# Optimization experiments

Hardware: AMD Instinct MI355X
Metric: run time of the kernel (lower is better)

## Reference

```python
import jax, jax.numpy as jnp
import numpy as np

B = 8192          # batch size
D = 128           # embedding_dim
R = 1000          # relation_dict_len
MARGIN = 1.0


def setup_inputs() -> dict:
    key = jax.random.key(0)
    k1, k2, k3, k4 = jax.random.split(key, 4)
    return {
        "positive_batch": jax.random.normal(k1, (B, 3, D), dtype=jnp.float32),
        "negative_batch": jax.random.normal(k2, (B, 3, D), dtype=jnp.float32),
        "r_idx": jax.random.randint(k3, (B,), 0, R),
        "rel_emb": jax.random.normal(k4, (R, D * D), dtype=jnp.float32),
    }


def _score(batch, Wr):
    # batch: (B, 3, D) -> h, r, t each (B, D); Wr: (B, D, D)
    h, r, t = batch[:, 0], batch[:, 1], batch[:, 2]
    d = jnp.abs(h + r - t)                       # (B, D)
    # x^T Wr x quadratic form per example, fused in one einsum
    return jnp.einsum('bi,bij,bj->b', d, Wr, d)  # (B,)


def reference(positive_batch, negative_batch, r_idx, rel_emb):
    # Gather per-example relation matrix (Wr built from positive relation,
    # reused for the negative score, as in the original module).
    Wr = rel_emb[r_idx].reshape(-1, D, D)        # (B, D, D)
    pos = _score(positive_batch, Wr)
    neg = _score(negative_batch, Wr)
    return jnp.mean(jax.nn.relu(MARGIN + pos - neg))
```

## Files before the change

### kernel.cpp

```cpp
#include <hip/hip_runtime.h>

#define BATCH 8192
#define DIM 128
#define NREL 1000
#define MARGIN 1.0f

#define WS_PARTIAL 0
#define WS_CNT     8192
#define WS_PSTART  9216
#define WS_CURSOR  10240
#define WS_ORDER   11264
#define ORDER_CAP  11264

__global__ __launch_bounds__(256) void init_kernel(int* __restrict__ cnt,
                                                   int* __restrict__ order) {
  int i = blockIdx.x * 256 + threadIdx.x;
  if (i < 1024) cnt[i] = 0;
  if (i < ORDER_CAP) order[i] = -1;
}

__global__ __launch_bounds__(256) void count_kernel(const int* __restrict__ r_idx,
                                                    int* __restrict__ cnt) {
  int i = blockIdx.x * 256 + threadIdx.x;
  if (i < BATCH) atomicAdd(&cnt[r_idx[i]], 1);
}

__global__ __launch_bounds__(256) void scan_kernel(const int* __restrict__ cnt,
                                                   int* __restrict__ pstart,
                                                   int* __restrict__ cursor) {
  int tid = threadIdx.x, lane = tid & 63, wave = tid >> 6;
  int base = tid * 4;
  int c[4], lsum = 0;
#pragma unroll
  for (int k = 0; k < 4; ++k) {
    int i = base + k;
    c[k] = (i < NREL) ? ((cnt[i] + 3) & ~3) : 0;
    lsum += c[k];
  }
  int v = lsum;
#pragma unroll
  for (int o = 1; o < 64; o <<= 1) {
    int u = __shfl_up(v, o, 64);
    if (lane >= o) v += u;
  }
  __shared__ int wsum[4];
  if (lane == 63) wsum[wave] = v;
  __syncthreads();
  int woff = 0;
  for (int w = 0; w < wave; ++w) woff += wsum[w];
  int toff = woff + v - lsum;
#pragma unroll
  for (int k = 0; k < 4; ++k) {
    int i = base + k;
    if (i < NREL) {
      pstart[i] = toff;
      cursor[i] = toff;
    }
    toff += c[k];
  }
}

__global__ __launch_bounds__(256) void scatter_kernel(const int* __restrict__ r_idx,
                                                      int* __restrict__ cursor,
                                                      int* __restrict__ order) {
  int i = blockIdx.x * 256 + threadIdx.x;
  if (i < BATCH) {
    int p = atomicAdd(&cursor[r_idx[i]], 1);
    order[p] = i;
  }
}

__device__ inline float2 dvec(const float* __restrict__ b, int c0) {
  float2 h = *(const float2*)(b + c0);
  float2 r = *(const float2*)(b + DIM + c0);
  float2 t = *(const float2*)(b + 2 * DIM + c0);
  return make_float2(fabsf(h.x + r.x - t.x), fabsf(h.y + r.y - t.y));
}

__global__ __launch_bounds__(256) void score_kernel(
    const float* __restrict__ pos_b, const float* __restrict__ neg_b,
    const int* __restrict__ r_idx, const float* __restrict__ rel_emb,
    const int* __restrict__ order, float* __restrict__ partial) {
  __shared__ float s_d[4][DIM][8];
  const int tid = threadIdx.x, lane = tid & 63, wave = tid >> 6;
  const int g4 = (blockIdx.x * 4 + wave) * 4;
  int4 es = *(const int4*)(order + g4);
  if (es.x < 0) return;
  const int c0 = lane * 2;
  const int r = r_idx[es.x];
  const bool v1 = es.y >= 0, v2 = es.z >= 0, v3 = es.w >= 0;
  const int e1 = v1 ? es.y : es.x, e2 = v2 ? es.z : es.x, e3 = v3 ? es.w : es.x;

  const float2 z = make_float2(0.f, 0.f);
  float2 dp0 = dvec(pos_b + (size_t)es.x * 3 * DIM, c0);
  float2 dn0 = dvec(neg_b + (size_t)es.x * 3 * DIM, c0);
  float2 dp1 = v1 ? dvec(pos_b + (size_t)e1 * 3 * DIM, c0) : z;
  float2 dn1 = v1 ? dvec(neg_b + (size_t)e1 * 3 * DIM, c0) : z;
  float2 dp2 = v2 ? dvec(pos_b + (size_t)e2 * 3 * DIM, c0) : z;
  float2 dn2 = v2 ? dvec(neg_b + (size_t)e2 * 3 * DIM, c0) : z;
  float2 dp3 = v3 ? dvec(pos_b + (size_t)e3 * 3 * DIM, c0) : z;
  float2 dn3 = v3 ? dvec(neg_b + (size_t)e3 * 3 * DIM, c0) : z;

  *(float4*)&s_d[wave][c0][0]     = make_float4(dp0.x, dp1.x, dp2.x, dp3.x);
  *(float4*)&s_d[wave][c0][4]     = make_float4(dn0.x, dn1.x, dn2.x, dn3.x);
  *(float4*)&s_d[wave][c0 + 1][0] = make_float4(dp0.y, dp1.y, dp2.y, dp3.y);
  *(float4*)&s_d[wave][c0 + 1][4] = make_float4(dn0.y, dn1.y, dn2.y, dn3.y);

  const float* W = rel_emb + (size_t)r * (DIM * DIM) + c0;
  float2 ap0 = z, ap1 = z, ap2 = z, ap3 = z;
  float2 an0 = z, an1 = z, an2 = z, an3 = z;
#pragma unroll 8
  for (int i = 0; i < DIM; ++i) {
    float2 wv = *(const float2*)(W + (size_t)i * DIM);
    float4 ddp = *(const float4*)&s_d[wave][i][0];
    float4 ddn = *(const float4*)&s_d[wave][i][4];
    ap0.x = fmaf(ddp.x, wv.x, ap0.x);  ap0.y = fmaf(ddp.x, wv.y, ap0.y);
    ap1.x = fmaf(ddp.y, wv.x, ap1.x);  ap1.y = fmaf(ddp.y, wv.y, ap1.y);
    ap2.x = fmaf(ddp.z, wv.x, ap2.x);  ap2.y = fmaf(ddp.z, wv.y, ap2.y);
    ap3.x = fmaf(ddp.w, wv.x, ap3.x);  ap3.y = fmaf(ddp.w, wv.y, ap3.y);
    an0.x = fmaf(ddn.x, wv.x, an0.x);  an0.y = fmaf(ddn.x, wv.y, an0.y);
    an1.x = fmaf(ddn.y, wv.x, an1.x);  an1.y = fmaf(ddn.y, wv.y, an1.y);
    an2.x = fmaf(ddn.z, wv.x, an2.x);  an2.y = fmaf(ddn.z, wv.y, an2.y);
    an3.x = fmaf(ddn.w, wv.x, an3.x);  an3.y = fmaf(ddn.w, wv.y, an3.y);
  }

  float s0 = ap0.x * dp0.x + ap0.y * dp0.y - an0.x * dn0.x - an0.y * dn0.y;
  float s1 = ap1.x * dp1.x + ap1.y * dp1.y - an1.x * dn1.x - an1.y * dn1.y;
  float s2 = ap2.x * dp2.x + ap2.y * dp2.y - an2.x * dn2.x - an2.y * dn2.y;
  float s3 = ap3.x * dp3.x + ap3.y * dp3.y - an3.x * dn3.x - an3.y * dn3.y;
#pragma unroll
  for (int o = 32; o > 0; o >>= 1) {
    s0 += __shfl_xor(s0, o, 64);
    s1 += __shfl_xor(s1, o, 64);
    s2 += __shfl_xor(s2, o, 64);
    s3 += __shfl_xor(s3, o, 64);
  }
  if (lane == 0) {
    partial[es.x] = s0;
    if (v1) partial[es.y] = s1;
    if (v2) partial[es.z] = s2;
    if (v3) partial[es.w] = s3;
  }
}

__global__ __launch_bounds__(256) void reduce_kernel(const float* __restrict__ partial,
                                                     float* __restrict__ out) {
  float acc = 0.f;
  for (int i = threadIdx.x; i < BATCH; i += 256) {
    float v = MARGIN + partial[i];
    acc += (v > 0.f) ? v : 0.f;
  }
#pragma unroll
  for (int o = 32; o > 0; o >>= 1) acc += __shfl_xor(acc, o, 64);
  __shared__ float s[4];
  const int lane = threadIdx.x & 63, wave = threadIdx.x >> 6;
  if (lane == 0) s[wave] = acc;
  __syncthreads();
  if (threadIdx.x == 0) out[0] = (s[0] + s[1] + s[2] + s[3]) * (1.0f / BATCH);
}

extern "C" void kernel_launch(void* const* d_in, const int* in_sizes, int n_in,
                              void* d_out, int out_size, void* d_ws, size_t ws_size,
                              hipStream_t stream) {
  const float* pos_b = (const float*)d_in[0];
  const float* neg_b = (const float*)d_in[1];
  const int* r_idx = (const int*)d_in[2];
  const float* rel_emb = (const float*)d_in[3];
  float* out = (float*)d_out;

  int* ws_i = (int*)d_ws;
  float* partial = (float*)d_ws + WS_PARTIAL;
  int* cnt = ws_i + WS_CNT;
  int* pstart = ws_i + WS_PSTART;
  int* cursor = ws_i + WS_CURSOR;
  int* order = ws_i + WS_ORDER;

  init_kernel<<<(ORDER_CAP + 255) / 256, 256, 0, stream>>>(cnt, order);
  count_kernel<<<BATCH / 256, 256, 0, stream>>>(r_idx, cnt);
  scan_kernel<<<1, 256, 0, stream>>>(cnt, pstart, cursor);
  scatter_kernel<<<BATCH / 256, 256, 0, stream>>>(r_idx, cursor, order);
  score_kernel<<<700, 256, 0, stream>>>(pos_b, neg_b, r_idx, rel_emb, order,
                                        partial);
  reduce_kernel<<<1, 256, 0, stream>>>(partial, out);
}
```

Before: 47.37 us.

## Fuse sort stages into one block and split relation rows across wave pairs

The four grouping kernels (init, count, scan, scatter) are merged into a single 1024-thread block that builds the order array with shared-memory atomics. This removes three launches and the global atomics. The score kernel now gives each 4-example group to two waves, each covering half of the 128 rows of W with float4 loads, and launches twice as many blocks. Each half writes its own partial buffer and the reduce kernel adds the two. The sort is serialized on one block, and each group's d vectors are now recomputed by both waves.

After: 46.45 us. Within noise of the previous version (-2.0%).

```diff
diff --git a/kernel.cpp b/kernel.cpp
--- a/kernel.cpp
+++ b/kernel.cpp
@@ -5,68 +5,44 @@
 #define NREL 1000
 #define MARGIN 1.0f
 
-#define WS_PARTIAL 0
-#define WS_CNT     8192
-#define WS_PSTART  9216
-#define WS_CURSOR  10240
-#define WS_ORDER   11264
-#define ORDER_CAP  11264
+#define WS_PA 0
+#define WS_PB 8192
+#define WS_ORDER 16384
+#define ORDER_CAP 11264
 
-__global__ __launch_bounds__(256) void init_kernel(int* __restrict__ cnt,
-                                                   int* __restrict__ order) {
-  int i = blockIdx.x * 256 + threadIdx.x;
-  if (i < 1024) cnt[i] = 0;
-  if (i < ORDER_CAP) order[i] = -1;
-}
-
-__global__ __launch_bounds__(256) void count_kernel(const int* __restrict__ r_idx,
-                                                    int* __restrict__ cnt) {
-  int i = blockIdx.x * 256 + threadIdx.x;
-  if (i < BATCH) atomicAdd(&cnt[r_idx[i]], 1);
-}
-
-__global__ __launch_bounds__(256) void scan_kernel(const int* __restrict__ cnt,
-                                                   int* __restrict__ pstart,
-                                                   int* __restrict__ cursor) {
-  int tid = threadIdx.x, lane = tid & 63, wave = tid >> 6;
-  int base = tid * 4;
-  int c[4], lsum = 0;
+__global__ __launch_bounds__(1024) void sort_kernel(const int* __restrict__ r_idx,
+                                                    int* __restrict__ order) {
+  __shared__ int s_cnt[1024];
+  __shared__ int s_cur[1024];
+  __shared__ int s_wsum[16];
+  const int tid = threadIdx.x, lane = tid & 63, wave = tid >> 6;
+  s_cnt[tid] = 0;
+  __syncthreads();
+  int my[8];
 #pragma unroll
-  for (int k = 0; k < 4; ++k) {
-    int i = base + k;
-    c[k] = (i < NREL) ? ((cnt[i] + 3) & ~3) : 0;
-    lsum += c[k];
+  for (int k = 0; k < 8; ++k) {
+    my[k] = r_idx[tid + k * 1024];
+    atomicAdd(&s_cnt[my[k]], 1);
   }
-  int v = lsum;
+  __syncthreads();
+  const int c = (s_cnt[tid] + 3) & ~3;
+  int v = c;
 #pragma unroll
   for (int o = 1; o < 64; o <<= 1) {
     int u = __shfl_up(v, o, 64);
     if (lane >= o) v += u;
   }
-  __shared__ int wsum[4];
-  if (lane == 63) wsum[wave] = v;
+  if (lane == 63) s_wsum[wave] = v;
   __syncthreads();
   int woff = 0;
-  for (int w = 0; w < wave; ++w) woff += wsum[w];
-  int toff = woff + v - lsum;
+  for (int w = 0; w < wave; ++w) woff += s_wsum[w];
+  s_cur[tid] = woff + v - c;
+  for (int i = tid; i < ORDER_CAP; i += 1024) order[i] = -1;
+  __syncthreads();
 #pragma unroll
-  for (int k = 0; k < 4; ++k) {
-    int i = base + k;
-    if (i < NREL) {
-      pstart[i] = toff;
-      cursor[i] = toff;
-    }
-    toff += c[k];
-  }
-}
-
-__global__ __launch_bounds__(256) void scatter_kernel(const int* __restrict__ r_idx,
-                                                      int* __restrict__ cursor,
-                                                      int* __restrict__ order) {
-  int i = blockIdx.x * 256 + threadIdx.x;
-  if (i < BATCH) {
-    int p = atomicAdd(&cursor[r_idx[i]], 1);
-    order[p] = i;
+  for (int k = 0; k < 8; ++k) {
+    int p = atomicAdd(&s_cur[my[k]], 1);
+    order[p] = tid + k * 1024;
   }
 }
 
@@ -80,11 +56,13 @@
 __global__ __launch_bounds__(256) void score_kernel(
     const float* __restrict__ pos_b, const float* __restrict__ neg_b,
     const int* __restrict__ r_idx, const float* __restrict__ rel_emb,
-    const int* __restrict__ order, float* __restrict__ partial) {
+    const int* __restrict__ order, float* __restrict__ pA,
+    float* __restrict__ pB) {
   __shared__ float s_d[4][DIM][8];
   const int tid = threadIdx.x, lane = tid & 63, wave = tid >> 6;
-  const int g4 = (blockIdx.x * 4 + wave) * 4;
-  int4 es = *(const int4*)(order + g4);
+  const int pair = wave >> 1, half = wave & 1;
+  const int g = blockIdx.x * 2 + pair;
+  int4 es = *(const int4*)(order + g * 4);
   if (es.x < 0) return;
   const int c0 = lane * 2;
   const int r = r_idx[es.x];
@@ -106,28 +84,52 @@
   *(float4*)&s_d[wave][c0 + 1][0] = make_float4(dp0.y, dp1.y, dp2.y, dp3.y);
   *(float4*)&s_d[wave][c0 + 1][4] = make_float4(dn0.y, dn1.y, dn2.y, dn3.y);
 
-  const float* W = rel_emb + (size_t)r * (DIM * DIM) + c0;
-  float2 ap0 = z, ap1 = z, ap2 = z, ap3 = z;
-  float2 an0 = z, an1 = z, an2 = z, an3 = z;
-#pragma unroll 8
-  for (int i = 0; i < DIM; ++i) {
-    float2 wv = *(const float2*)(W + (size_t)i * DIM);
-    float4 ddp = *(const float4*)&s_d[wave][i][0];
-    float4 ddn = *(const float4*)&s_d[wave][i][4];
-    ap0.x = fmaf(ddp.x, wv.x, ap0.x);  ap0.y = fmaf(ddp.x, wv.y, ap0.y);
-    ap1.x = fmaf(ddp.y, wv.x, ap1.x);  ap1.y = fmaf(ddp.y, wv.y, ap1.y);
-    ap2.x = fmaf(ddp.z, wv.x, ap2.x);  ap2.y = fmaf(ddp.z, wv.y, ap2.y);
-    ap3.x = fmaf(ddp.w, wv.x, ap3.x);  ap3.y = fmaf(ddp.w, wv.y, ap3.y);
-    an0.x = fmaf(ddn.x, wv.x, an0.x);  an0.y = fmaf(ddn.x, wv.y, an0.y);
-    an1.x = fmaf(ddn.y, wv.x, an1.x);  an1.y = fmaf(ddn.y, wv.y, an1.y);
-    an2.x = fmaf(ddn.z, wv.x, an2.x);  an2.y = fmaf(ddn.z, wv.y, an2.y);
-    an3.x = fmaf(ddn.w, wv.x, an3.x);  an3.y = fmaf(ddn.w, wv.y, an3.y);
+  const int colb = (lane & 31) * 4;
+  const int rsel = lane >> 5;
+  const int rowbase = half * 64;
+  const float* W = rel_emb + (size_t)r * (DIM * DIM) +
+                   (size_t)(rowbase + rsel) * DIM + colb;
+
+  float4 fz = make_float4(0.f, 0.f, 0.f, 0.f);
+  float4 ap0 = fz, ap1 = fz, ap2 = fz, ap3 = fz;
+  float4 an0 = fz, an1 = fz, an2 = fz, an3 = fz;
+#pragma unroll 4
+  for (int it = 0; it < 32; ++it) {
+    float4 wv = *(const float4*)(W + (size_t)(it * 2) * DIM);
+    const int row = rowbase + it * 2 + rsel;
+    float4 ddp = *(const float4*)&s_d[wave][row][0];
+    float4 ddn = *(const float4*)&s_d[wave][row][4];
+    ap0.x = fmaf(ddp.x, wv.x, ap0.x); ap0.y = fmaf(ddp.x, wv.y, ap0.y);
+    ap0.z = fmaf(ddp.x, wv.z, ap0.z); ap0.w = fmaf(ddp.x, wv.w, ap0.w);
+    ap1.x = fmaf(ddp.y, wv.x, ap1.x); ap1.y = fmaf(ddp.y, wv.y, ap1.y);
+    ap1.z = fmaf(ddp.y, wv.z, ap1.z); ap1.w = fmaf(ddp.y, wv.w, ap1.w);
+    ap2.x = fmaf(ddp.z, wv.x, ap2.x); ap2.y = fmaf(ddp.z, wv.y, ap2.y);
+    ap2.z = fmaf(ddp.z, wv.z, ap2.z); ap2.w = fmaf(ddp.z, wv.w, ap2.w);
+    ap3.x = fmaf(ddp.w, wv.x, ap3.x); ap3.y = fmaf(ddp.w, wv.y, ap3.y);
+    ap3.z = fmaf(ddp.w, wv.z, ap3.z); ap3.w = fmaf(ddp.w, wv.w, ap3.w);
+    an0.x = fmaf(ddn.x, wv.x, an0.x); an0.y = fmaf(ddn.x, wv.y, an0.y);
+    an0.z = fmaf(ddn.x, wv.z, an0.z); an0.w = fmaf(ddn.x, wv.w, an0.w);
+    an1.x = fmaf(ddn.y, wv.x, an1.x); an1.y = fmaf(ddn.y, wv.y, an1.y);
+    an1.z = fmaf(ddn.y, wv.z, an1.z); an1.w = fmaf(ddn.y, wv.w, an1.w);
+    an2.x = fmaf(ddn.z, wv.x, an2.x); an2.y = fmaf(ddn.z, wv.y, an2.y);
+    an2.z = fmaf(ddn.z, wv.z, an2.z); an2.w = fmaf(ddn.z, wv.w, an2.w);
+    an3.x = fmaf(ddn.w, wv.x, an3.x); an3.y = fmaf(ddn.w, wv.y, an3.y);
+    an3.z = fmaf(ddn.w, wv.z, an3.z); an3.w = fmaf(ddn.w, wv.w, an3.w);
   }
 
-  float s0 = ap0.x * dp0.x + ap0.y * dp0.y - an0.x * dn0.x - an0.y * dn0.y;
-  float s1 = ap1.x * dp1.x + ap1.y * dp1.y - an1.x * dn1.x - an1.y * dn1.y;
-  float s2 = ap2.x * dp2.x + ap2.y * dp2.y - an2.x * dn2.x - an2.y * dn2.y;
-  float s3 = ap3.x * dp3.x + ap3.y * dp3.y - an3.x * dn3.x - an3.y * dn3.y;
+  float s0 = 0.f, s1 = 0.f, s2 = 0.f, s3 = 0.f;
+#define EPI(K, COMP)                                          \
+  {                                                           \
+    float4 dp4 = *(const float4*)&s_d[wave][colb + K][0];     \
+    float4 dn4 = *(const float4*)&s_d[wave][colb + K][4];     \
+    s0 += ap0.COMP * dp4.x - an0.COMP * dn4.x;                \
+    s1 += ap1.COMP * dp4.y - an1.COMP * dn4.y;                \
+    s2 += ap2.COMP * dp4.z - an2.COMP * dn4.z;                \
+    s3 += ap3.COMP * dp4.w - an3.COMP * dn4.w;                \
+  }
+  EPI(0, x) EPI(1, y) EPI(2, z) EPI(3, w)
+#undef EPI
+
 #pragma unroll
   for (int o = 32; o > 0; o >>= 1) {
     s0 += __shfl_xor(s0, o, 64);
@@ -135,19 +137,21 @@
     s2 += __shfl_xor(s2, o, 64);
     s3 += __shfl_xor(s3, o, 64);
   }
+  float* P = half ? pB : pA;
   if (lane == 0) {
-    partial[es.x] = s0;
-    if (v1) partial[es.y] = s1;
-    if (v2) partial[es.z] = s2;
-    if (v3) partial[es.w] = s3;
+    P[es.x] = s0;
+    if (v1) P[es.y] = s1;
+    if (v2) P[es.z] = s2;
+    if (v3) P[es.w] = s3;
   }
 }
 
-__global__ __launch_bounds__(256) void reduce_kernel(const float* __restrict__ partial,
+__global__ __launch_bounds__(256) void reduce_kernel(const float* __restrict__ pA,
+                                                     const float* __restrict__ pB,
                                                      float* __restrict__ out) {
   float acc = 0.f;
   for (int i = threadIdx.x; i < BATCH; i += 256) {
-    float v = MARGIN + partial[i];
+    float v = MARGIN + pA[i] + pB[i];
     acc += (v > 0.f) ? v : 0.f;
   }
 #pragma unroll
@@ -168,18 +172,12 @@
   const float* rel_emb = (const float*)d_in[3];
   float* out = (float*)d_out;
 
-  int* ws_i = (int*)d_ws;
-  float* partial = (float*)d_ws + WS_PARTIAL;
-  int* cnt = ws_i + WS_CNT;
-  int* pstart = ws_i + WS_PSTART;
-  int* cursor = ws_i + WS_CURSOR;
-  int* order = ws_i + WS_ORDER;
+  float* pA = (float*)d_ws + WS_PA;
+  float* pB = (float*)d_ws + WS_PB;
+  int* order = (int*)d_ws + WS_ORDER;
 
-  init_kernel<<<(ORDER_CAP + 255) / 256, 256, 0, stream>>>(cnt, order);
-  count_kernel<<<BATCH / 256, 256, 0, stream>>>(r_idx, cnt);
-  scan_kernel<<<1, 256, 0, stream>>>(cnt, pstart, cursor);
-  scatter_kernel<<<BATCH / 256, 256, 0, stream>>>(r_idx, cursor, order);
-  score_kernel<<<700, 256, 0, stream>>>(pos_b, neg_b, r_idx, rel_emb, order,
-                                        partial);
-  reduce_kernel<<<1, 256, 0, stream>>>(partial, out);
+  sort_kernel<<<1, 1024, 0, stream>>>(r_idx, order);
+  score_kernel<<<1400, 256, 0, stream>>>(pos_b, neg_b, r_idx, rel_emb, order,
+                                         pA, pB);
+  reduce_kernel<<<1, 256, 0, stream>>>(pA, pB, out);
 }
```
